# Optimization experiments

Measured on AMD Instinct MI355X. Metric: run time of the kernel, lower is better.

## Reference

```python
import jax, jax.numpy as jnp
import numpy as np

EPS = 1e-5
STD = 0.02  # BERT initializer_range


def _bn(x, g, b):
    # BatchNorm1d in training mode: batch stats, biased variance
    m = jnp.mean(x, axis=0)
    v = jnp.mean((x - m) ** 2, axis=0)
    return g * (x - m) / jnp.sqrt(v + EPS) + b


def _gcn(x, src, dst, deg_isqrt, W, b, N):
    norm = deg_isqrt[src] * deg_isqrt[dst]
    msg = (x @ W)[src] * norm[:, None]
    return jax.ops.segment_sum(msg, dst, num_segments=N) + b


def setup_inputs() -> dict:
    key = jax.random.key(0)
    ks = jax.random.split(key, 24)
    B, S, E = 64, 512, 768
    D = E // 2            # 384, embed_size_gnn
    NG = 512              # nodes per graph
    N = B * NG            # 32768 total nodes
    Edges = 1048576
    C = 3                 # num_classes

    inp = {}
    inp["last_h"] = jax.random.normal(ks[0], (B, S, E), jnp.float32)
    inp["first_h"] = jax.random.normal(ks[1], (B, S, E), jnp.float32)
    inp["x_nodes"] = jax.random.normal(ks[2], (N, 300), jnp.float32)
    inp["edge_index"] = jax.random.randint(ks[3], (2, Edges), 0, N, jnp.int32)

    # exactly 2 masked nodes per sample (model reshapes to [B, 2, D])
    rng = np.random.default_rng(0)
    mask = np.zeros((B, NG), np.int32)
    for i in range(B):
        pos = rng.choice(NG, size=2, replace=False)
        mask[i, pos] = 1
    inp["graph_masking"] = jnp.asarray(mask)

    # params (stored [in, out]; torch Linear is [out, in])
    inp["w_pre1"] = STD * jax.random.normal(ks[4], (300, D), jnp.float32)
    inp["b_pre1"] = jnp.zeros((D,), jnp.float32)
    inp["w_pre2"] = STD * jax.random.normal(ks[5], (D, D), jnp.float32)
    inp["b_pre2"] = jnp.zeros((D,), jnp.float32)
    inp["w_conv"] = STD * jax.random.normal(ks[6], (3, D, D), jnp.float32)
    inp["b_conv"] = jnp.zeros((3, D), jnp.float32)
    inp["bng_g"] = jnp.ones((7, D), jnp.float32)
    inp["bng_b"] = jnp.zeros((7, D), jnp.float32)
    inp["w_post1"] = STD * jax.random.normal(ks[7], (D, D), jnp.float32)
    inp["b_post1"] = jnp.zeros((D,), jnp.float32)
    inp["w_post2"] = STD * jax.random.normal(ks[8], (D, D), jnp.float32)
    inp["b_post2"] = jnp.zeros((D,), jnp.float32)
    inp["w_cat"] = STD * jax.random.normal(ks[9], (E, E), jnp.float32)
    inp["b_cat"] = jnp.zeros((E,), jnp.float32)
    inp["bn_g"] = jnp.ones((2, E), jnp.float32)
    inp["bn_b"] = jnp.zeros((2, E), jnp.float32)
    inp["w_out"] = STD * jax.random.normal(ks[10], (E, C), jnp.float32)
    inp["b_out"] = jnp.zeros((C,), jnp.float32)
    return inp


def reference(last_h, first_h, x_nodes, edge_index, graph_masking,
              w_pre1, b_pre1, w_pre2, b_pre2, w_conv, b_conv, bng_g, bng_b,
              w_post1, b_post1, w_post2, b_post2, w_cat, b_cat, bn_g, bn_b,
              w_out, b_out):
    relu = jax.nn.relu
    B, NG = graph_masking.shape
    N = x_nodes.shape[0]

    # sentence branch: first/last hidden-state average, mean pool
    H_sent = jnp.mean(0.5 * (last_h + first_h), axis=1)  # [B, E]

    # GNN pre-MLPs
    x = _bn(relu(x_nodes @ w_pre1 + b_pre1), bng_g[0], bng_b[0])
    x = _bn(relu(x @ w_pre2 + b_pre2), bng_g[1], bng_b[1])

    # self-loop-augmented edge list, degree norm (shared across convs)
    loop = jnp.arange(N, dtype=edge_index.dtype)
    src = jnp.concatenate([edge_index[0], loop])
    dst = jnp.concatenate([edge_index[1], loop])
    deg = jax.ops.segment_sum(jnp.ones_like(dst, jnp.float32), dst, num_segments=N)
    deg_isqrt = jax.lax.rsqrt(deg)

    out = x
    for i in range(3):
        out = _bn(relu(_gcn(x, src, dst, deg_isqrt, w_conv[i], b_conv[i], N)),
                  bng_g[i + 2], bng_b[i + 2])

    out = _bn(relu(out @ w_post1 + b_post1), bng_g[5], bng_b[5])
    out = _bn(relu(out @ w_post2 + b_post2), bng_g[6], bng_b[6])  # [N, D]

    # reshape_graph_embeddings: gather the 2 masked nodes per sample
    # nodes are laid out contiguously per graph (NG nodes each)
    _, sel = jax.lax.top_k(graph_masking, 2)           # [B, 2] local idx, ascending on ties
    gidx = jnp.arange(B)[:, None] * NG + sel            # global node idx
    nodes = out[gidx]                                   # [B, 2, D]
    flat = nodes.reshape(B, -1)                         # [B, E]

    outc = _bn(relu(flat @ w_cat + b_cat), bn_g[0], bn_b[0])
    att = _bn(H_sent, bn_g[1], bn_b[1]) + outc
    return att @ w_out + b_out                          # [B, num_classes]
```

## Files before the change

### kernel.cpp

```cpp
#include <hip/hip_runtime.h>

typedef unsigned int uint32;
typedef unsigned short ushort16;

typedef __attribute__((ext_vector_type(8))) short bf16x8;
typedef __attribute__((ext_vector_type(4))) float f32x4;

#define NNODES 32768
#define DFEAT 384
#define KPAD1 320

__device__ __forceinline__ float bf2f(ushort16 u) {
  union { uint32 i; float f; } x; x.i = ((uint32)u) << 16; return x.f;
}
__device__ __forceinline__ float bflo(uint32 v) {
  union { uint32 i; float f; } x; x.i = v << 16; return x.f;
}
__device__ __forceinline__ float bfhi(uint32 v) {
  union { uint32 i; float f; } x; x.i = v & 0xffff0000u; return x.f;
}
__device__ __forceinline__ ushort16 f2bf(float f) {
  union { float f; uint32 i; } x; x.f = f;
  uint32 r = (x.i + 0x7fffu + ((x.i >> 16) & 1u)) >> 16;
  return (ushort16)r;
}

__global__ void convert_x_kernel(const float* __restrict__ X, ushort16* __restrict__ A0) {
  int row = blockIdx.x * 4 + (threadIdx.x >> 6);
  int lane = threadIdx.x & 63;
  const float* xr = X + (size_t)row * 300;
  ushort16* ar = A0 + (size_t)row * KPAD1;
#pragma unroll
  for (int i = 0; i < 5; ++i) {
    int col = lane + i * 64;
    float v = (col < 300) ? xr[col] : 0.f;
    ar[col] = f2bf(v);
  }
}

__global__ void sent_mean_kernel(const float* __restrict__ last,
                                 const float* __restrict__ first,
                                 float* __restrict__ Hpart) {
  int b = blockIdx.x, sc = blockIdx.y, e = threadIdx.x;
  int s0 = sc * 32;
  const float* pl = last + ((size_t)b * 512 + s0) * 768 + e;
  const float* pf = first + ((size_t)b * 512 + s0) * 768 + e;
  float a0 = 0.f, a1 = 0.f, a2 = 0.f, a3 = 0.f;
  for (int i = 0; i < 32; i += 4) {
    a0 += pl[(i + 0) * 768] + pf[(i + 0) * 768];
    a1 += pl[(i + 1) * 768] + pf[(i + 1) * 768];
    a2 += pl[(i + 2) * 768] + pf[(i + 2) * 768];
    a3 += pl[(i + 3) * 768] + pf[(i + 3) * 768];
  }
  Hpart[((size_t)sc * 64 + b) * 768 + e] = a0 + a1 + a2 + a3;
}
__global__ void hsent_kernel(const float* __restrict__ Hpart, float* __restrict__ Hsent) {
  int b = blockIdx.x, e = threadIdx.x;
  float h = 0.f;
#pragma unroll
  for (int sc = 0; sc < 16; ++sc) h += Hpart[((size_t)sc * 64 + b) * 768 + e];
  Hsent[(size_t)b * 768 + e] = h * (0.5f / 512.f);
}

__global__ void deg_count_kernel(const int* __restrict__ dst, int* __restrict__ cnt, int E) {
  int e = blockIdx.x * blockDim.x + threadIdx.x;
  if (e < E) atomicAdd(&cnt[dst[e]], 1);
}
__global__ void disq_kernel(const int* __restrict__ cnt, float* __restrict__ disq) {
  int n = blockIdx.x * blockDim.x + threadIdx.x;
  if (n < NNODES) disq[n] = rsqrtf((float)cnt[n] + 1.0f);
}
__global__ void scan_kernel(const int* __restrict__ cnt, int* __restrict__ row_start,
                            int* __restrict__ cursor) {
  __shared__ int buf[1024];
  int t = threadIdx.x;
  int base = t * 32;
  int s = 0;
  for (int i = 0; i < 32; ++i) s += cnt[base + i];
  buf[t] = s; __syncthreads();
  int x = s;
  for (int off = 1; off < 1024; off <<= 1) {
    int v = (t >= off) ? buf[t - off] : 0;
    __syncthreads();
    x += v; buf[t] = x;
    __syncthreads();
  }
  int run = x - s;
  for (int i = 0; i < 32; ++i) {
    row_start[base + i] = run; cursor[base + i] = run;
    run += cnt[base + i];
  }
  if (t == 1023) row_start[NNODES] = run;
}
__global__ void scatter_kernel(const int* __restrict__ src, const int* __restrict__ dst,
                               int* __restrict__ cursor, int* __restrict__ csr, int E) {
  int e = blockIdx.x * blockDim.x + threadIdx.x;
  if (e < E) {
    int d = dst[e];
    int pos = atomicAdd(&cursor[d], 1);
    csr[pos] = src[e];
  }
}

__global__ void xform_w_kernel(const float* __restrict__ W, const float* __restrict__ bias,
                               const float* __restrict__ stat, const float* __restrict__ g,
                               const float* __restrict__ bb, float invN,
                               ushort16* __restrict__ BT, float* __restrict__ bias_out,
                               int K, int Kpad, int Nw) {
  __shared__ float red[128];
  int n = blockIdx.x, t = threadIdx.x;
  float part = 0.f;
  for (int k = t; k < Kpad; k += 128) {
    ushort16 o = 0; float contrib = 0.f;
    if (k < K) {
      float ak = 1.f, shk = 0.f;
      if (stat) {
        float s = 0.f, q = 0.f;
        for (int i = 0; i < 8; ++i) { s += stat[k * 8 + i]; q += stat[(DFEAT + k) * 8 + i]; }
        float mean = s * invN, var = q * invN - mean * mean;
        ak = g[k] * rsqrtf(var + 1e-5f);
        shk = bb[k] - ak * mean;
      }
      float w = W[(size_t)k * Nw + n];
      o = f2bf(ak * w);
      contrib = shk * w;
    }
    BT[(size_t)n * Kpad + k] = o;
    part += contrib;
  }
  red[t] = part; __syncthreads();
  for (int off = 64; off > 0; off >>= 1) {
    if (t < off) red[t] += red[t + off];
    __syncthreads();
  }
  if (t == 0) bias_out[n] = (bias ? bias[n] : 0.f) + red[0];
}

#define BM 128
#define BN 128
#define BKT 32
#define LDT 40

template <bool RELU, bool STATS, bool RSCALE>
__global__ __launch_bounds__(256) void gemm_bf16(
    const ushort16* __restrict__ A, int lda, const ushort16* __restrict__ BT, int ldb,
    const float* __restrict__ bias, const float* __restrict__ rowscale,
    ushort16* __restrict__ C, int Ntot, int K, float* __restrict__ stat) {
  __shared__ __attribute__((aligned(16))) ushort16 As[BM * LDT];
  __shared__ __attribute__((aligned(16))) ushort16 Bs[BN * LDT];
  __shared__ float ssum[BN], ssq[BN];
  int bm0 = blockIdx.x * BM, bn0 = blockIdx.y * BN;
  int tid = threadIdx.x;
  if (STATS) {
    if (tid < BN) { ssum[tid] = 0.f; ssq[tid] = 0.f; }
  }
  int lane = tid & 63, wave = tid >> 6;
  int wm = (wave & 1) * 64, wn = (wave >> 1) * 64;
  int l15 = lane & 15, quad = lane >> 4;

  f32x4 acc[4][4];
  for (int i = 0; i < 4; ++i)
    for (int j = 0; j < 4; ++j) acc[i][j] = (f32x4)0.f;

  for (int kk = 0; kk < K; kk += BKT) {
    __syncthreads();
    for (int i = 0; i < 2; ++i) {
      int chunk = tid + i * 256;
      int row = chunk >> 2, cc = chunk & 3;
      uint4 va = *(const uint4*)(A + (size_t)(bm0 + row) * lda + kk + cc * 8);
      *(uint4*)(&As[row * LDT + cc * 8]) = va;
      uint4 vb = *(const uint4*)(BT + (size_t)(bn0 + row) * ldb + kk + cc * 8);
      *(uint4*)(&Bs[row * LDT + cc * 8]) = vb;
    }
    __syncthreads();
    bf16x8 af[4], bfr[4];
    for (int mi = 0; mi < 4; ++mi)
      af[mi] = *(const bf16x8*)(&As[(wm + mi * 16 + l15) * LDT + quad * 8]);
    for (int ni = 0; ni < 4; ++ni)
      bfr[ni] = *(const bf16x8*)(&Bs[(wn + ni * 16 + l15) * LDT + quad * 8]);
    for (int mi = 0; mi < 4; ++mi)
      for (int ni = 0; ni < 4; ++ni)
        acc[mi][ni] = __builtin_amdgcn_mfma_f32_16x16x32_bf16(af[mi], bfr[ni], acc[mi][ni], 0, 0, 0);
  }
  for (int ni = 0; ni < 4; ++ni) {
    int coll = wn + ni * 16 + l15;
    int col = bn0 + coll;
    float bv = bias[col];
    float s = 0.f, q = 0.f;
    for (int mi = 0; mi < 4; ++mi) {
      for (int r = 0; r < 4; ++r) {
        int row = bm0 + wm + mi * 16 + quad * 4 + r;
        float v = acc[mi][ni][r] + bv;
        if (RELU) v = fmaxf(v, 0.f);
        if (RSCALE) v *= rowscale[row];
        C[(size_t)row * Ntot + col] = f2bf(v);
        if (STATS) { s += v; q += v * v; }
      }
    }
    if (STATS) { atomicAdd(&ssum[coll], s); atomicAdd(&ssq[coll], q); }
  }
  if (STATS) {
    __syncthreads();
    int sp = blockIdx.x & 7;
    if (tid < BN) {
      atomicAdd(&stat[(bn0 + tid) * 8 + sp], ssum[tid]);
      atomicAdd(&stat[(DFEAT + bn0 + tid) * 8 + sp], ssq[tid]);
    }
  }
}

__global__ __launch_bounds__(256) void aggregate_kernel(
    const uint32* __restrict__ XWs, const int* __restrict__ csr,
    const int* __restrict__ row_start, const float* __restrict__ disq,
    const float* __restrict__ bconv, uint32* __restrict__ RC2,
    float* __restrict__ stat) {
  int bx = blockIdx.x;
  int slot = bx & 7, g = bx >> 3;
  int chunk = slot < 6 ? slot : (slot == 6 ? 0 : 3);
  int noff = slot < 6 ? 0 : 16384;
  int ngrp = (slot == 0 || slot == 3 || slot >= 6) ? 512 : 1024;
  if (g >= ngrp) return;
  __shared__ float ssum[64], ssq[64];
  int tid = threadIdx.x;
  if (tid < 64) { ssum[tid] = 0.f; ssq[tid] = 0.f; }
  __syncthreads();
  int lane = tid & 63, wave = tid >> 6;
  int half = lane >> 5, cl = lane & 31;
  int hb = half << 5;
  int cbase = chunk * 32;
  float b0 = bconv[chunk * 64 + 2 * cl], b1 = bconv[chunk * 64 + 2 * cl + 1];
  float ls0 = 0.f, ls1 = 0.f, lq0 = 0.f, lq1 = 0.f;
  int nodebase = noff + (g * 4 + wave) * 8;
  for (int ni = 0; ni < 8; ++ni) {
    int n = nodebase + ni;
    int beg = row_start[n], end = row_start[n + 1];
    int deg = end - beg;
    int len0 = (deg + 1) >> 1;
    int myBeg = beg + (half ? len0 : 0);
    int myLen = half ? (deg - len0) : len0;
    float a0, a1;
    if (half == 0) {
      uint32 v = XWs[(size_t)n * 192 + cbase + cl];
      a0 = bflo(v); a1 = bfhi(v);
    } else { a0 = 0.f; a1 = 0.f; }
    for (int bb0 = 0; bb0 < len0; bb0 += 32) {
      int rem = myLen - bb0;
      int idx = (cl < rem) ? csr[myBeg + bb0 + cl] : -1;
      int jmax = min(32, len0 - bb0);
      int j = 0;
      for (; j + 8 <= jmax; j += 8) {
        uint32 v[8];
#pragma unroll
        for (int jj = 0; jj < 8; ++jj) {
          int s = __shfl(idx, hb + j + jj, 64);
          int sa = (s < 0) ? 0 : s;
          uint32 m = (s < 0) ? 0u : 0xffffffffu;
          v[jj] = XWs[(size_t)sa * 192 + cbase + cl] & m;
        }
#pragma unroll
        for (int jj = 0; jj < 8; ++jj) { a0 += bflo(v[jj]); a1 += bfhi(v[jj]); }
      }
      for (; j < jmax; ++j) {
        int s = __shfl(idx, hb + j, 64);
        int sa = (s < 0) ? 0 : s;
        uint32 m = (s < 0) ? 0u : 0xffffffffu;
        uint32 v = XWs[(size_t)sa * 192 + cbase + cl] & m;
        a0 += bflo(v); a1 += bfhi(v);
      }
    }
    a0 += __shfl_xor(a0, 32, 64);
    a1 += __shfl_xor(a1, 32, 64);
    if (half == 0) {
      float din = disq[n];
      a0 = fmaxf(din * a0 + b0, 0.f);
      a1 = fmaxf(din * a1 + b1, 0.f);
      RC2[(size_t)n * 192 + cbase + cl] = (uint32)f2bf(a0) | ((uint32)f2bf(a1) << 16);
      ls0 += a0; lq0 += a0 * a0; ls1 += a1; lq1 += a1 * a1;
    }
  }
  if (half == 0) {
    atomicAdd(&ssum[2 * cl], ls0); atomicAdd(&ssum[2 * cl + 1], ls1);
    atomicAdd(&ssq[2 * cl], lq0);  atomicAdd(&ssq[2 * cl + 1], lq1);
  }
  __syncthreads();
  if (tid < 64) {
    int col = chunk * 64 + tid;
    int sp = g & 7;
    atomicAdd(&stat[col * 8 + sp], ssum[tid]);
    atomicAdd(&stat[(DFEAT + col) * 8 + sp], ssq[tid]);
  }
}

__global__ void gather_kernel(const int* __restrict__ mask, const ushort16* __restrict__ R5,
                              const float* __restrict__ stat, const float* __restrict__ g,
                              const float* __restrict__ bb, float invN,
                              float* __restrict__ flat) {
  __shared__ int smin, smax;
  int b = blockIdx.x, t = threadIdx.x;
  if (t == 0) { smin = 1 << 30; smax = -1; }
  __syncthreads();
  for (int p = t; p < 512; p += 384)
    if (mask[b * 512 + p]) { atomicMin(&smin, p); atomicMax(&smax, p); }
  __syncthreads();
  float s = 0.f, q = 0.f;
  for (int i = 0; i < 8; ++i) { s += stat[t * 8 + i]; q += stat[(DFEAT + t) * 8 + i]; }
  float mean = s * invN, var = q * invN - mean * mean;
  float a = g[t] * rsqrtf(var + 1e-5f), sh = bb[t] - a * mean;
  int sel[2] = {smin, smax};
  for (int j = 0; j < 2; ++j) {
    float v = bf2f(R5[(size_t)(b * 512 + sel[j]) * DFEAT + t]);
    flat[(size_t)b * 768 + j * DFEAT + t] = a * v + sh;
  }
}

__global__ void cat_gemm_kernel(const float* __restrict__ flat, const float* __restrict__ Wc,
                                const float* __restrict__ bc, float* __restrict__ out) {
  int t = threadIdx.x;
  int j = blockIdx.x * 64 + (t & 63);
  int b = blockIdx.y * 16 + (t >> 6);
  const float* fr = flat + (size_t)b * 768;
  float acc = bc[j];
#pragma unroll 4
  for (int k = 0; k < 768; ++k) acc += fr[k] * Wc[(size_t)k * 768 + j];
  out[(size_t)b * 768 + j] = fmaxf(acc, 0.f);
}
__global__ void bnstats_kernel(const float* __restrict__ catrelu, const float* __restrict__ Hsent,
                               const float* __restrict__ g, const float* __restrict__ bb,
                               float* __restrict__ aff) {
  int c = blockIdx.x * 64 + threadIdx.x;
  float s1 = 0, q1 = 0, s2 = 0, q2 = 0;
  for (int b = 0; b < 64; ++b) {
    float v = catrelu[b * 768 + c]; s1 += v; q1 += v * v;
    float h = Hsent[b * 768 + c];   s2 += h; q2 += h * h;
  }
  const float inv = 1.0f / 64.0f;
  float m1 = s1 * inv, var1 = q1 * inv - m1 * m1;
  float a1 = g[c] * rsqrtf(var1 + 1e-5f);
  aff[c] = a1; aff[768 + c] = bb[c] - a1 * m1;
  float m2 = s2 * inv, var2 = q2 * inv - m2 * m2;
  float a2 = g[768 + c] * rsqrtf(var2 + 1e-5f);
  aff[1536 + c] = a2; aff[2304 + c] = bb[768 + c] - a2 * m2;
}
__global__ void final_kernel(const float* __restrict__ Hs, const float* __restrict__ catrelu,
                             const float* __restrict__ aff, const float* __restrict__ w_out,
                             const float* __restrict__ b_out, float* __restrict__ out) {
  __shared__ float red[12];
  int b = blockIdx.x, t = threadIdx.x;
  float p0 = 0, p1 = 0, p2 = 0;
  for (int k = t; k < 768; k += 256) {
    float att = (aff[1536 + k] * Hs[b * 768 + k] + aff[2304 + k]) +
                (aff[k] * catrelu[b * 768 + k] + aff[768 + k]);
    p0 += att * w_out[k * 3 + 0];
    p1 += att * w_out[k * 3 + 1];
    p2 += att * w_out[k * 3 + 2];
  }
  for (int off = 32; off > 0; off >>= 1) {
    p0 += __shfl_down(p0, off, 64);
    p1 += __shfl_down(p1, off, 64);
    p2 += __shfl_down(p2, off, 64);
  }
  int wv = t >> 6;
  if ((t & 63) == 0) { red[wv * 3 + 0] = p0; red[wv * 3 + 1] = p1; red[wv * 3 + 2] = p2; }
  __syncthreads();
  if (t == 0) {
    out[b * 3 + 0] = b_out[0] + red[0] + red[3] + red[6] + red[9];
    out[b * 3 + 1] = b_out[1] + red[1] + red[4] + red[7] + red[10];
    out[b * 3 + 2] = b_out[2] + red[2] + red[5] + red[8] + red[11];
  }
}

extern "C" void kernel_launch(void* const* d_in, const int* in_sizes, int n_in,
                              void* d_out, int out_size, void* d_ws, size_t ws_size,
                              hipStream_t stream) {
  const float* last_h  = (const float*)d_in[0];
  const float* first_h = (const float*)d_in[1];
  const float* x_nodes = (const float*)d_in[2];
  const int*   edges   = (const int*)d_in[3];
  const int*   mask    = (const int*)d_in[4];
  const float* w_pre1  = (const float*)d_in[5];
  const float* b_pre1  = (const float*)d_in[6];
  const float* w_pre2  = (const float*)d_in[7];
  const float* b_pre2  = (const float*)d_in[8];
  const float* w_conv  = (const float*)d_in[9];
  const float* b_conv  = (const float*)d_in[10];
  const float* bng_g   = (const float*)d_in[11];
  const float* bng_b   = (const float*)d_in[12];
  const float* w_post1 = (const float*)d_in[13];
  const float* b_post1 = (const float*)d_in[14];
  const float* w_post2 = (const float*)d_in[15];
  const float* b_post2 = (const float*)d_in[16];
  const float* w_cat   = (const float*)d_in[17];
  const float* b_cat   = (const float*)d_in[18];
  const float* bn_g    = (const float*)d_in[19];
  const float* bn_b    = (const float*)d_in[20];
  const float* w_out   = (const float*)d_in[21];
  const float* b_out   = (const float*)d_in[22];
  float* out = (float*)d_out;

  const int E = in_sizes[3] / 2;
  const int* e_src = edges;
  const int* e_dst = edges + E;

  char* w = (char*)d_ws;
  size_t off = 0;
  auto alloc = [&](size_t bytes) { size_t p = off; off = (off + bytes + 255) & ~(size_t)255; return p; };
  ushort16* buf0   = (ushort16*)(w + alloc((size_t)NNODES * DFEAT * 2));
  ushort16* buf1   = (ushort16*)(w + alloc((size_t)NNODES * DFEAT * 2));
  int*    csr      = (int*)(w + alloc((size_t)E * 4));
  int*    rowstart = (int*)(w + alloc((size_t)(NNODES + 1) * 4));
  int*    cursor   = (int*)(w + alloc((size_t)NNODES * 4));
  float*  disq     = (float*)(w + alloc((size_t)NNODES * 4));
  ushort16* BT     = (ushort16*)(w + alloc((size_t)DFEAT * DFEAT * 2));
  float*  biasx    = (float*)(w + alloc(DFEAT * 4));
  float*  flat     = (float*)(w + alloc(64 * 768 * 4));
  float*  catrelu  = (float*)(w + alloc(64 * 768 * 4));
  float*  aff64    = (float*)(w + alloc(4 * 768 * 4));
  float*  Hpart    = (float*)(w + alloc((size_t)16 * 64 * 768 * 4));
  float*  Hsent    = (float*)(w + alloc(64 * 768 * 4));
  size_t zoff = off;
  int*   degcnt = (int*)(w + alloc((size_t)NNODES * 4));
  float* stats  = (float*)(w + alloc((size_t)5 * 768 * 8 * 4));
  size_t zbytes = off - zoff;

  hipMemsetAsync(w + zoff, 0, zbytes, stream);

  const float invN = 1.0f / (float)NNODES;
  float* st0 = stats + 0 * 768 * 8;
  float* st1 = stats + 1 * 768 * 8;
  float* st2 = stats + 2 * 768 * 8;
  float* st3 = stats + 3 * 768 * 8;
  float* st4 = stats + 4 * 768 * 8;

  convert_x_kernel<<<NNODES / 4, 256, 0, stream>>>(x_nodes, buf0);
  xform_w_kernel<<<DFEAT, 128, 0, stream>>>(w_pre1, b_pre1, nullptr, nullptr, nullptr, invN, BT, biasx, 300, KPAD1, DFEAT);
  sent_mean_kernel<<<dim3(64, 16), 768, 0, stream>>>(last_h, first_h, Hpart);
  hsent_kernel<<<64, 768, 0, stream>>>(Hpart, Hsent);
  deg_count_kernel<<<(E + 255) / 256, 256, 0, stream>>>(e_dst, degcnt, E);
  disq_kernel<<<NNODES / 256, 256, 0, stream>>>(degcnt, disq);
  scan_kernel<<<1, 1024, 0, stream>>>(degcnt, rowstart, cursor);
  scatter_kernel<<<(E + 255) / 256, 256, 0, stream>>>(e_src, e_dst, cursor, csr, E);

  dim3 ggrid(NNODES / BM, DFEAT / BN);

  gemm_bf16<true, true, false><<<ggrid, 256, 0, stream>>>(buf0, KPAD1, BT, KPAD1, biasx, nullptr, buf1, DFEAT, KPAD1, st0);
  xform_w_kernel<<<DFEAT, 128, 0, stream>>>(w_pre2, b_pre2, st0, bng_g + 0 * DFEAT, bng_b + 0 * DFEAT, invN, BT, biasx, DFEAT, DFEAT, DFEAT);

  gemm_bf16<true, true, false><<<ggrid, 256, 0, stream>>>(buf1, DFEAT, BT, DFEAT, biasx, nullptr, buf0, DFEAT, DFEAT, st1);
  xform_w_kernel<<<DFEAT, 128, 0, stream>>>(w_conv + 2 * DFEAT * DFEAT, nullptr, st1, bng_g + 1 * DFEAT, bng_b + 1 * DFEAT, invN, BT, biasx, DFEAT, DFEAT, DFEAT);

  gemm_bf16<false, false, true><<<ggrid, 256, 0, stream>>>(buf0, DFEAT, BT, DFEAT, biasx, disq, buf1, DFEAT, DFEAT, nullptr);

  aggregate_kernel<<<8192, 256, 0, stream>>>((const uint32*)buf1, csr, rowstart, disq, b_conv + 2 * DFEAT, (uint32*)buf0, st2);
  xform_w_kernel<<<DFEAT, 128, 0, stream>>>(w_post1, b_post1, st2, bng_g + 4 * DFEAT, bng_b + 4 * DFEAT, invN, BT, biasx, DFEAT, DFEAT, DFEAT);

  gemm_bf16<true, true, false><<<ggrid, 256, 0, stream>>>(buf0, DFEAT, BT, DFEAT, biasx, nullptr, buf1, DFEAT, DFEAT, st3);
  xform_w_kernel<<<DFEAT, 128, 0, stream>>>(w_post2, b_post2, st3, bng_g + 5 * DFEAT, bng_b + 5 * DFEAT, invN, BT, biasx, DFEAT, DFEAT, DFEAT);

  gemm_bf16<true, true, false><<<ggrid, 256, 0, stream>>>(buf1, DFEAT, BT, DFEAT, biasx, nullptr, buf0, DFEAT, DFEAT, st4);

  gather_kernel<<<64, DFEAT, 0, stream>>>(mask, buf0, st4, bng_g + 6 * DFEAT, bng_b + 6 * DFEAT, invN, flat);
  cat_gemm_kernel<<<dim3(12, 4), 1024, 0, stream>>>(flat, w_cat, b_cat, catrelu);
  bnstats_kernel<<<12, 64, 0, stream>>>(catrelu, Hsent, bn_g, bn_b, aff64);
  final_kernel<<<64, 256, 0, stream>>>(Hsent, catrelu, aff64, w_out, b_out, out);
}
```

Measured before the change: 910.0 us.

## Fuse small kernels, retile weight transform, rebalance aggregation, merge gather with cat GEMM

Several unrelated changes land together. The hsent, disq and gather kernels are folded into neighbouring kernels (bnstats, scan, and a combined catgather+cat GEMM), which cuts launches and intermediate buffers. The weight transform now transposes through a shared-memory tile so that W reads are coalesced, using 6 blocks instead of 384. The aggregation is rewritten to give each wave one lane per feature pair, with a contiguous node range balanced across slots, and CSR now stores pre-multiplied row offsets. The sentence-mean split is made coarser. Risks include lower parallelism in the weight transform and cat GEMM, and load imbalance from high-degree nodes in the aggregation.

```diff
diff --git a/kernel.cpp b/kernel.cpp
--- a/kernel.cpp
+++ b/kernel.cpp
@@ -42,11 +42,11 @@
                                  const float* __restrict__ first,
                                  float* __restrict__ Hpart) {
   int b = blockIdx.x, sc = blockIdx.y, e = threadIdx.x;
-  int s0 = sc * 32;
+  int s0 = sc * 128;
   const float* pl = last + ((size_t)b * 512 + s0) * 768 + e;
   const float* pf = first + ((size_t)b * 512 + s0) * 768 + e;
   float a0 = 0.f, a1 = 0.f, a2 = 0.f, a3 = 0.f;
-  for (int i = 0; i < 32; i += 4) {
+  for (int i = 0; i < 128; i += 4) {
     a0 += pl[(i + 0) * 768] + pf[(i + 0) * 768];
     a1 += pl[(i + 1) * 768] + pf[(i + 1) * 768];
     a2 += pl[(i + 2) * 768] + pf[(i + 2) * 768];
@@ -54,29 +54,19 @@
   }
   Hpart[((size_t)sc * 64 + b) * 768 + e] = a0 + a1 + a2 + a3;
 }
-__global__ void hsent_kernel(const float* __restrict__ Hpart, float* __restrict__ Hsent) {
-  int b = blockIdx.x, e = threadIdx.x;
-  float h = 0.f;
-#pragma unroll
-  for (int sc = 0; sc < 16; ++sc) h += Hpart[((size_t)sc * 64 + b) * 768 + e];
-  Hsent[(size_t)b * 768 + e] = h * (0.5f / 512.f);
-}
 
 __global__ void deg_count_kernel(const int* __restrict__ dst, int* __restrict__ cnt, int E) {
   int e = blockIdx.x * blockDim.x + threadIdx.x;
   if (e < E) atomicAdd(&cnt[dst[e]], 1);
 }
-__global__ void disq_kernel(const int* __restrict__ cnt, float* __restrict__ disq) {
-  int n = blockIdx.x * blockDim.x + threadIdx.x;
-  if (n < NNODES) disq[n] = rsqrtf((float)cnt[n] + 1.0f);
-}
 __global__ void scan_kernel(const int* __restrict__ cnt, int* __restrict__ row_start,
-                            int* __restrict__ cursor) {
+                            int* __restrict__ cursor, float* __restrict__ disq) {
   __shared__ int buf[1024];
   int t = threadIdx.x;
   int base = t * 32;
+  int lc[32];
   int s = 0;
-  for (int i = 0; i < 32; ++i) s += cnt[base + i];
+  for (int i = 0; i < 32; ++i) { lc[i] = cnt[base + i]; s += lc[i]; }
   buf[t] = s; __syncthreads();
   int x = s;
   for (int off = 1; off < 1024; off <<= 1) {
@@ -88,7 +78,8 @@
   int run = x - s;
   for (int i = 0; i < 32; ++i) {
     row_start[base + i] = run; cursor[base + i] = run;
-    run += cnt[base + i];
+    disq[base + i] = rsqrtf((float)lc[i] + 1.0f);
+    run += lc[i];
   }
   if (t == 1023) row_start[NNODES] = run;
 }
@@ -98,7 +89,7 @@
   if (e < E) {
     int d = dst[e];
     int pos = atomicAdd(&cursor[d], 1);
-    csr[pos] = src[e];
+    csr[pos] = src[e] * 192;
   }
 }
 
@@ -106,34 +97,51 @@
                                const float* __restrict__ stat, const float* __restrict__ g,
                                const float* __restrict__ bb, float invN,
                                ushort16* __restrict__ BT, float* __restrict__ bias_out,
-                               int K, int Kpad, int Nw) {
-  __shared__ float red[128];
-  int n = blockIdx.x, t = threadIdx.x;
+                               int K, int Kpad) {
+  __shared__ float tile[64 * 65];
+  __shared__ float la[64], lsh[64];
+  __shared__ float psum[4][64];
+  const int Nw = DFEAT;
+  int n0 = blockIdx.x * 64;
+  int t = threadIdx.x;
+  int nn = t & 63, r = t >> 6;
   float part = 0.f;
-  for (int k = t; k < Kpad; k += 128) {
-    ushort16 o = 0; float contrib = 0.f;
-    if (k < K) {
-      float ak = 1.f, shk = 0.f;
-      if (stat) {
-        float s = 0.f, q = 0.f;
-        for (int i = 0; i < 8; ++i) { s += stat[k * 8 + i]; q += stat[(DFEAT + k) * 8 + i]; }
-        float mean = s * invN, var = q * invN - mean * mean;
-        ak = g[k] * rsqrtf(var + 1e-5f);
-        shk = bb[k] - ak * mean;
+  for (int k0 = 0; k0 < Kpad; k0 += 64) {
+    if (t < 64) {
+      int k = k0 + t;
+      float ak = 0.f, shk = 0.f;
+      if (k < K) {
+        ak = 1.f;
+        if (stat) {
+          float s = 0.f, q = 0.f;
+          for (int i = 0; i < 8; ++i) { s += stat[k * 8 + i]; q += stat[(DFEAT + k) * 8 + i]; }
+          float mean = s * invN, var = q * invN - mean * mean;
+          ak = g[k] * rsqrtf(var + 1e-5f);
+          shk = bb[k] - ak * mean;
+        }
       }
-      float w = W[(size_t)k * Nw + n];
-      o = f2bf(ak * w);
-      contrib = shk * w;
-    }
-    BT[(size_t)n * Kpad + k] = o;
-    part += contrib;
-  }
-  red[t] = part; __syncthreads();
-  for (int off = 64; off > 0; off >>= 1) {
-    if (t < off) red[t] += red[t + off];
-    __syncthreads();
-  }
-  if (t == 0) bias_out[n] = (bias ? bias[n] : 0.f) + red[0];
+      la[t] = ak; lsh[t] = shk;
+    }
+    __syncthreads();
+    for (int rr = r; rr < 64; rr += 4) {
+      int k = k0 + rr;
+      tile[rr * 65 + nn] = (k < K) ? W[(size_t)k * Nw + n0 + nn] : 0.f;
+    }
+    __syncthreads();
+    for (int i = 0; i < 16; ++i) {
+      int kk = r + 4 * i;
+      float w = tile[kk * 65 + nn];
+      BT[(size_t)(n0 + nn) * Kpad + k0 + kk] = f2bf(la[kk] * w);
+      part += lsh[kk] * w;
+    }
+    __syncthreads();
+  }
+  psum[r][nn] = part;
+  __syncthreads();
+  if (t < 64) {
+    bias_out[n0 + t] = (bias ? bias[n0 + t] : 0.f) +
+                       psum[0][t] + psum[1][t] + psum[2][t] + psum[3][t];
+  }
 }
 
 #define BM 128
@@ -209,6 +217,7 @@
   }
 }
 
+#define AGG_BPS 128
 __global__ __launch_bounds__(256) void aggregate_kernel(
     const uint32* __restrict__ XWs, const int* __restrict__ csr,
     const int* __restrict__ row_start, const float* __restrict__ disq,
@@ -216,122 +225,124 @@
     float* __restrict__ stat) {
   int bx = blockIdx.x;
   int slot = bx & 7, g = bx >> 3;
-  int chunk = slot < 6 ? slot : (slot == 6 ? 0 : 3);
-  int noff = slot < 6 ? 0 : 16384;
-  int ngrp = (slot == 0 || slot == 3 || slot >= 6) ? 512 : 1024;
-  if (g >= ngrp) return;
-  __shared__ float ssum[64], ssq[64];
-  int tid = threadIdx.x;
-  if (tid < 64) { ssum[tid] = 0.f; ssq[tid] = 0.f; }
+  int wave = __builtin_amdgcn_readfirstlane((int)(threadIdx.x >> 6));
+  int lane = threadIdx.x & 63;
+  int seg_chunk[2], seg_start[2], seg_cnt[2];
+  int nseg;
+  if (slot < 6) {
+    int m = slot / 3, part = slot % 3;
+    seg_chunk[0] = m;
+    seg_start[0] = part * 10923;
+    seg_cnt[0] = (part == 2) ? 10922 : 10923;
+    seg_chunk[1] = 2;
+    seg_start[1] = slot * 1365;
+    seg_cnt[1] = 1365;
+    nseg = 2;
+  } else {
+    seg_chunk[0] = 2;
+    seg_start[0] = 8190 + (slot - 6) * 12289;
+    seg_cnt[0] = 12289;
+    nseg = 1;
+  }
+  int vtot = seg_cnt[0] + ((nseg > 1) ? seg_cnt[1] : 0);
+  int tw = AGG_BPS * 4;
+  int wid = g * 4 + wave;
+  int per = (vtot + tw - 1) / tw;
+  int v0 = wid * per, v1 = min(vtot, v0 + per);
+  int segbase = 0;
+  for (int si = 0; si < nseg; ++si) {
+    int s0 = max(v0 - segbase, 0);
+    int s1 = min(v1 - segbase, seg_cnt[si]);
+    segbase += seg_cnt[si];
+    if (s0 >= s1) continue;
+    int chunk = seg_chunk[si];
+    const uint32* __restrict__ XWc = XWs + chunk * 64;
+    int c0 = chunk * 128 + 2 * lane;
+    float bias0 = bconv[c0], bias1 = bconv[c0 + 1];
+    float ss0 = 0.f, ss1 = 0.f, qq0 = 0.f, qq1 = 0.f;
+    int nA = seg_start[si] + s0, nB = seg_start[si] + s1;
+    for (int n = nA; n < nB; ++n) {
+      int beg = row_start[n], end = row_start[n + 1];
+      uint32 v = XWc[(size_t)n * 192 + lane];
+      float a0 = bflo(v), a1 = bfhi(v);
+      int j = beg;
+      for (; j + 8 <= end; j += 8) {
+        uint32 w[8];
+#pragma unroll
+        for (int t = 0; t < 8; ++t) w[t] = XWc[(size_t)(uint32)csr[j + t] + lane];
+#pragma unroll
+        for (int t = 0; t < 8; ++t) { a0 += bflo(w[t]); a1 += bfhi(w[t]); }
+      }
+      for (; j < end; ++j) {
+        uint32 w = XWc[(size_t)(uint32)csr[j] + lane];
+        a0 += bflo(w); a1 += bfhi(w);
+      }
+      float dn = disq[n];
+      a0 = fmaxf(fmaf(dn, a0, bias0), 0.f);
+      a1 = fmaxf(fmaf(dn, a1, bias1), 0.f);
+      RC2[(size_t)n * 192 + chunk * 64 + lane] = (uint32)f2bf(a0) | ((uint32)f2bf(a1) << 16);
+      ss0 += a0; qq0 += a0 * a0; ss1 += a1; qq1 += a1 * a1;
+    }
+    int sp = g & 7;
+    atomicAdd(&stat[c0 * 8 + sp], ss0);
+    atomicAdd(&stat[(DFEAT + c0) * 8 + sp], qq0);
+    atomicAdd(&stat[(c0 + 1) * 8 + sp], ss1);
+    atomicAdd(&stat[(DFEAT + c0 + 1) * 8 + sp], qq1);
+  }
+}
+
+__global__ __launch_bounds__(1024) void catgather_kernel(
+    const int* __restrict__ mask, const ushort16* __restrict__ R5,
+    const float* __restrict__ stat, const float* __restrict__ g6,
+    const float* __restrict__ b6, float invN,
+    const float* __restrict__ Wc, const float* __restrict__ bc,
+    float* __restrict__ catrelu) {
+  __shared__ float frow[8][768];
+  __shared__ int smin[8], smax[8];
+  int t = threadIdx.x;
+  int jt = blockIdx.x, bt = blockIdx.y;
+  if (t < 8) { smin[t] = 1 << 30; smax[t] = -1; }
   __syncthreads();
-  int lane = tid & 63, wave = tid >> 6;
-  int half = lane >> 5, cl = lane & 31;
-  int hb = half << 5;
-  int cbase = chunk * 32;
-  float b0 = bconv[chunk * 64 + 2 * cl], b1 = bconv[chunk * 64 + 2 * cl + 1];
-  float ls0 = 0.f, ls1 = 0.f, lq0 = 0.f, lq1 = 0.f;
-  int nodebase = noff + (g * 4 + wave) * 8;
-  for (int ni = 0; ni < 8; ++ni) {
-    int n = nodebase + ni;
-    int beg = row_start[n], end = row_start[n + 1];
-    int deg = end - beg;
-    int len0 = (deg + 1) >> 1;
-    int myBeg = beg + (half ? len0 : 0);
-    int myLen = half ? (deg - len0) : len0;
-    float a0, a1;
-    if (half == 0) {
-      uint32 v = XWs[(size_t)n * 192 + cbase + cl];
-      a0 = bflo(v); a1 = bfhi(v);
-    } else { a0 = 0.f; a1 = 0.f; }
-    for (int bb0 = 0; bb0 < len0; bb0 += 32) {
-      int rem = myLen - bb0;
-      int idx = (cl < rem) ? csr[myBeg + bb0 + cl] : -1;
-      int jmax = min(32, len0 - bb0);
-      int j = 0;
-      for (; j + 8 <= jmax; j += 8) {
-        uint32 v[8];
-#pragma unroll
-        for (int jj = 0; jj < 8; ++jj) {
-          int s = __shfl(idx, hb + j + jj, 64);
-          int sa = (s < 0) ? 0 : s;
-          uint32 m = (s < 0) ? 0u : 0xffffffffu;
-          v[jj] = XWs[(size_t)sa * 192 + cbase + cl] & m;
-        }
-#pragma unroll
-        for (int jj = 0; jj < 8; ++jj) { a0 += bflo(v[jj]); a1 += bfhi(v[jj]); }
-      }
-      for (; j < jmax; ++j) {
-        int s = __shfl(idx, hb + j, 64);
-        int sa = (s < 0) ? 0 : s;
-        uint32 m = (s < 0) ? 0u : 0xffffffffu;
-        uint32 v = XWs[(size_t)sa * 192 + cbase + cl] & m;
-        a0 += bflo(v); a1 += bfhi(v);
-      }
-    }
-    a0 += __shfl_xor(a0, 32, 64);
-    a1 += __shfl_xor(a1, 32, 64);
-    if (half == 0) {
-      float din = disq[n];
-      a0 = fmaxf(din * a0 + b0, 0.f);
-      a1 = fmaxf(din * a1 + b1, 0.f);
-      RC2[(size_t)n * 192 + cbase + cl] = (uint32)f2bf(a0) | ((uint32)f2bf(a1) << 16);
-      ls0 += a0; lq0 += a0 * a0; ls1 += a1; lq1 += a1 * a1;
-    }
-  }
-  if (half == 0) {
-    atomicAdd(&ssum[2 * cl], ls0); atomicAdd(&ssum[2 * cl + 1], ls1);
-    atomicAdd(&ssq[2 * cl], lq0);  atomicAdd(&ssq[2 * cl + 1], lq1);
+  for (int idx = t; idx < 8 * 512; idx += 1024) {
+    int bl = idx >> 9, p = idx & 511;
+    if (mask[(bt * 8 + bl) * 512 + p]) { atomicMin(&smin[bl], p); atomicMax(&smax[bl], p); }
   }
   __syncthreads();
-  if (tid < 64) {
-    int col = chunk * 64 + tid;
-    int sp = g & 7;
-    atomicAdd(&stat[col * 8 + sp], ssum[tid]);
-    atomicAdd(&stat[(DFEAT + col) * 8 + sp], ssq[tid]);
-  }
-}
-
-__global__ void gather_kernel(const int* __restrict__ mask, const ushort16* __restrict__ R5,
-                              const float* __restrict__ stat, const float* __restrict__ g,
-                              const float* __restrict__ bb, float invN,
-                              float* __restrict__ flat) {
-  __shared__ int smin, smax;
-  int b = blockIdx.x, t = threadIdx.x;
-  if (t == 0) { smin = 1 << 30; smax = -1; }
+  if (t < 768) {
+    int cp = (t >= 384) ? t - 384 : t;
+    int j = (t >= 384) ? 1 : 0;
+    float s = 0.f, q = 0.f;
+    for (int i = 0; i < 8; ++i) { s += stat[cp * 8 + i]; q += stat[(DFEAT + cp) * 8 + i]; }
+    float mean = s * invN, var = q * invN - mean * mean;
+    float a = g6[cp] * rsqrtf(var + 1e-5f), sh = b6[cp] - a * mean;
+    for (int bl = 0; bl < 8; ++bl) {
+      int gb = bt * 8 + bl;
+      int sel = j ? smax[bl] : smin[bl];
+      frow[bl][t] = a * bf2f(R5[(size_t)(gb * 512 + sel) * DFEAT + cp]) + sh;
+    }
+  }
   __syncthreads();
-  for (int p = t; p < 512; p += 384)
-    if (mask[b * 512 + p]) { atomicMin(&smin, p); atomicMax(&smax, p); }
-  __syncthreads();
-  float s = 0.f, q = 0.f;
-  for (int i = 0; i < 8; ++i) { s += stat[t * 8 + i]; q += stat[(DFEAT + t) * 8 + i]; }
-  float mean = s * invN, var = q * invN - mean * mean;
-  float a = g[t] * rsqrtf(var + 1e-5f), sh = bb[t] - a * mean;
-  int sel[2] = {smin, smax};
-  for (int j = 0; j < 2; ++j) {
-    float v = bf2f(R5[(size_t)(b * 512 + sel[j]) * DFEAT + t]);
-    flat[(size_t)b * 768 + j * DFEAT + t] = a * v + sh;
-  }
-}
-
-__global__ void cat_gemm_kernel(const float* __restrict__ flat, const float* __restrict__ Wc,
-                                const float* __restrict__ bc, float* __restrict__ out) {
-  int t = threadIdx.x;
-  int j = blockIdx.x * 64 + (t & 63);
-  int b = blockIdx.y * 16 + (t >> 6);
-  const float* fr = flat + (size_t)b * 768;
-  float acc = bc[j];
+  int jj = jt * 128 + (t & 127), bl = t >> 7;
+  float acc = bc[jj];
+  const float* fr = frow[bl];
 #pragma unroll 4
-  for (int k = 0; k < 768; ++k) acc += fr[k] * Wc[(size_t)k * 768 + j];
-  out[(size_t)b * 768 + j] = fmaxf(acc, 0.f);
-}
-__global__ void bnstats_kernel(const float* __restrict__ catrelu, const float* __restrict__ Hsent,
+  for (int k = 0; k < 768; ++k) acc = fmaf(fr[k], Wc[(size_t)k * 768 + jj], acc);
+  catrelu[(size_t)(bt * 8 + bl) * 768 + jj] = fmaxf(acc, 0.f);
+}
+
+__global__ void bnstats_kernel(const float* __restrict__ catrelu, const float* __restrict__ Hpart,
+                               float* __restrict__ Hsent,
                                const float* __restrict__ g, const float* __restrict__ bb,
                                float* __restrict__ aff) {
   int c = blockIdx.x * 64 + threadIdx.x;
   float s1 = 0, q1 = 0, s2 = 0, q2 = 0;
   for (int b = 0; b < 64; ++b) {
     float v = catrelu[b * 768 + c]; s1 += v; q1 += v * v;
-    float h = Hsent[b * 768 + c];   s2 += h; q2 += h * h;
+    float h = Hpart[((size_t)0 * 64 + b) * 768 + c] + Hpart[((size_t)1 * 64 + b) * 768 + c] +
+              Hpart[((size_t)2 * 64 + b) * 768 + c] + Hpart[((size_t)3 * 64 + b) * 768 + c];
+    h *= (0.5f / 512.f);
+    Hsent[(size_t)b * 768 + c] = h;
+    s2 += h; q2 += h * h;
   }
   const float inv = 1.0f / 64.0f;
   float m1 = s1 * inv, var1 = q1 * inv - m1 * m1;
@@ -341,6 +352,7 @@
   float a2 = g[768 + c] * rsqrtf(var2 + 1e-5f);
   aff[1536 + c] = a2; aff[2304 + c] = bb[768 + c] - a2 * m2;
 }
+
 __global__ void final_kernel(const float* __restrict__ Hs, const float* __restrict__ catrelu,
                              const float* __restrict__ aff, const float* __restrict__ w_out,
                              const float* __restrict__ b_out, float* __restrict__ out) {
@@ -412,10 +424,9 @@
   float*  disq     = (float*)(w + alloc((size_t)NNODES * 4));
   ushort16* BT     = (ushort16*)(w + alloc((size_t)DFEAT * DFEAT * 2));
   float*  biasx    = (float*)(w + alloc(DFEAT * 4));
-  float*  flat     = (float*)(w + alloc(64 * 768 * 4));
   float*  catrelu  = (float*)(w + alloc(64 * 768 * 4));
   float*  aff64    = (float*)(w + alloc(4 * 768 * 4));
-  float*  Hpart    = (float*)(w + alloc((size_t)16 * 64 * 768 * 4));
+  float*  Hpart    = (float*)(w + alloc((size_t)4 * 64 * 768 * 4));
   float*  Hsent    = (float*)(w + alloc(64 * 768 * 4));
   size_t zoff = off;
   int*   degcnt = (int*)(w + alloc((size_t)NNODES * 4));
@@ -432,34 +443,31 @@
   float* st4 = stats + 4 * 768 * 8;
 
   convert_x_kernel<<<NNODES / 4, 256, 0, stream>>>(x_nodes, buf0);
-  xform_w_kernel<<<DFEAT, 128, 0, stream>>>(w_pre1, b_pre1, nullptr, nullptr, nullptr, invN, BT, biasx, 300, KPAD1, DFEAT);
-  sent_mean_kernel<<<dim3(64, 16), 768, 0, stream>>>(last_h, first_h, Hpart);
-  hsent_kernel<<<64, 768, 0, stream>>>(Hpart, Hsent);
+  xform_w_kernel<<<6, 256, 0, stream>>>(w_pre1, b_pre1, nullptr, nullptr, nullptr, invN, BT, biasx, 300, KPAD1);
+  sent_mean_kernel<<<dim3(64, 4), 768, 0, stream>>>(last_h, first_h, Hpart);
   deg_count_kernel<<<(E + 255) / 256, 256, 0, stream>>>(e_dst, degcnt, E);
-  disq_kernel<<<NNODES / 256, 256, 0, stream>>>(degcnt, disq);
-  scan_kernel<<<1, 1024, 0, stream>>>(degcnt, rowstart, cursor);
+  scan_kernel<<<1, 1024, 0, stream>>>(degcnt, rowstart, cursor, disq);
   scatter_kernel<<<(E + 255) / 256, 256, 0, stream>>>(e_src, e_dst, cursor, csr, E);
 
   dim3 ggrid(NNODES / BM, DFEAT / BN);
 
   gemm_bf16<true, true, false><<<ggrid, 256, 0, stream>>>(buf0, KPAD1, BT, KPAD1, biasx, nullptr, buf1, DFEAT, KPAD1, st0);
-  xform_w_kernel<<<DFEAT, 128, 0, stream>>>(w_pre2, b_pre2, st0, bng_g + 0 * DFEAT, bng_b + 0 * DFEAT, invN, BT, biasx, DFEAT, DFEAT, DFEAT);
+  xform_w_kernel<<<6, 256, 0, stream>>>(w_pre2, b_pre2, st0, bng_g + 0 * DFEAT, bng_b + 0 * DFEAT, invN, BT, biasx, DFEAT, DFEAT);
 
   gemm_bf16<true, true, false><<<ggrid, 256, 0, stream>>>(buf1, DFEAT, BT, DFEAT, biasx, nullptr, buf0, DFEAT, DFEAT, st1);
-  xform_w_kernel<<<DFEAT, 128, 0, stream>>>(w_conv + 2 * DFEAT * DFEAT, nullptr, st1, bng_g + 1 * DFEAT, bng_b + 1 * DFEAT, invN, BT, biasx, DFEAT, DFEAT, DFEAT);
+  xform_w_kernel<<<6, 256, 0, stream>>>(w_conv + 2 * DFEAT * DFEAT, nullptr, st1, bng_g + 1 * DFEAT, bng_b + 1 * DFEAT, invN, BT, biasx, DFEAT, DFEAT);
 
   gemm_bf16<false, false, true><<<ggrid, 256, 0, stream>>>(buf0, DFEAT, BT, DFEAT, biasx, disq, buf1, DFEAT, DFEAT, nullptr);
 
-  aggregate_kernel<<<8192, 256, 0, stream>>>((const uint32*)buf1, csr, rowstart, disq, b_conv + 2 * DFEAT, (uint32*)buf0, st2);
-  xform_w_kernel<<<DFEAT, 128, 0, stream>>>(w_post1, b_post1, st2, bng_g + 4 * DFEAT, bng_b + 4 * DFEAT, invN, BT, biasx, DFEAT, DFEAT, DFEAT);
+  aggregate_kernel<<<8 * AGG_BPS, 256, 0, stream>>>((const uint32*)buf1, csr, rowstart, disq, b_conv + 2 * DFEAT, (uint32*)buf0, st2);
+  xform_w_kernel<<<6, 256, 0, stream>>>(w_post1, b_post1, st2, bng_g + 4 * DFEAT, bng_b + 4 * DFEAT, invN, BT, biasx, DFEAT, DFEAT);
 
   gemm_bf16<true, true, false><<<ggrid, 256, 0, stream>>>(buf0, DFEAT, BT, DFEAT, biasx, nullptr, buf1, DFEAT, DFEAT, st3);
-  xform_w_kernel<<<DFEAT, 128, 0, stream>>>(w_post2, b_post2, st3, bng_g + 5 * DFEAT, bng_b + 5 * DFEAT, invN, BT, biasx, DFEAT, DFEAT, DFEAT);
+  xform_w_kernel<<<6, 256, 0, stream>>>(w_post2, b_post2, st3, bng_g + 5 * DFEAT, bng_b + 5 * DFEAT, invN, BT, biasx, DFEAT, DFEAT);
 
   gemm_bf16<true, true, false><<<ggrid, 256, 0, stream>>>(buf1, DFEAT, BT, DFEAT, biasx, nullptr, buf0, DFEAT, DFEAT, st4);
 
-  gather_kernel<<<64, DFEAT, 0, stream>>>(mask, buf0, st4, bng_g + 6 * DFEAT, bng_b + 6 * DFEAT, invN, flat);
-  cat_gemm_kernel<<<dim3(12, 4), 1024, 0, stream>>>(flat, w_cat, b_cat, catrelu);
-  bnstats_kernel<<<12, 64, 0, stream>>>(catrelu, Hsent, bn_g, bn_b, aff64);
+  catgather_kernel<<<dim3(6, 8), 1024, 0, stream>>>(mask, buf0, st4, bng_g + 6 * DFEAT, bng_b + 6 * DFEAT, invN, w_cat, b_cat, catrelu);
+  bnstats_kernel<<<12, 64, 0, stream>>>(catrelu, Hpart, Hsent, bn_g, bn_b, aff64);
   final_kernel<<<64, 256, 0, stream>>>(Hsent, catrelu, aff64, w_out, b_out, out);
 }
```

Measured after the change: 1.200 ms. 31.9% more time.
